# Performance work log

Hardware: AMD Instinct MI355X
Metric: run time of the kernel (lower is better)

## Reference

```python
import jax, jax.numpy as jnp
import numpy as np

C = 256
CQK = C // 8  # 32


def setup_inputs() -> dict:
    key = jax.random.key(0)
    ks = jax.random.split(key, 7)
    x = jax.random.normal(ks[0], (4, C, 64, 64), dtype=jnp.float32)
    s = 1.0 / np.sqrt(C)
    Wq = jax.random.normal(ks[1], (CQK, C), dtype=jnp.float32) * s
    bq = jnp.zeros((CQK,), dtype=jnp.float32)
    Wk = jax.random.normal(ks[2], (CQK, C), dtype=jnp.float32) * s
    bk = jnp.zeros((CQK,), dtype=jnp.float32)
    Wv = jax.random.normal(ks[3], (C, C), dtype=jnp.float32) * s
    bv = jnp.zeros((C,), dtype=jnp.float32)
    return {"x": x, "Wq": Wq, "bq": bq, "Wk": Wk, "bk": bk, "Wv": Wv, "bv": bv}


def reference(x, Wq, bq, Wk, bk, Wv, bv):
    B, Cc, H, W = x.shape
    xf = x.reshape(B, Cc, H * W)  # [B, C, HW]
    # 1x1 convs == per-pixel linear projections over channels
    q = jnp.einsum('oc,bcn->bno', Wq, xf) + bq          # [B, HW, C//8]
    k = jnp.einsum('oc,bcn->bon', Wk, xf) + bk[:, None]  # [B, C//8, HW]
    v = jnp.einsum('oc,bcn->bno', Wv, xf) + bv          # [B, HW, C]
    attn = jax.nn.softmax(jnp.einsum('bnd,bdm->bnm', q, k), axis=-1)  # [B, HW, HW]
    out = jnp.einsum('bnm,bmc->bnc', attn, v)           # [B, HW, C]
    return out.transpose(0, 2, 1).reshape(B, Cc, H, W)
```

## Files before the change

kernel.cpp:

```cpp
#include <hip/hip_runtime.h>
#include <hip/hip_bf16.h>


#define N_PIX 4096
#define DQK   32
#define CCH   256
#define LOG2E 1.44269504088896f

typedef __attribute__((ext_vector_type(8))) _Float16 f16x8;
typedef __attribute__((ext_vector_type(4))) _Float16 f16x4;
typedef __attribute__((ext_vector_type(2))) _Float16 f16x2;
typedef __attribute__((ext_vector_type(8))) short    bf16x8;
typedef __attribute__((ext_vector_type(4))) short    bf16x4;
typedef __attribute__((ext_vector_type(4))) float    f32x4;

__device__ inline void barrier_lds() {
    asm volatile("" ::: "memory");
    __builtin_amdgcn_s_waitcnt(0xc07f);
    __builtin_amdgcn_s_barrier();
    asm volatile("" ::: "memory");
}

__device__ inline unsigned cvt_pk_bf16(float lo, float hi) {
    unsigned r;
    asm("v_cvt_pk_bf16_f32 %0, %1, %2" : "=v"(r) : "v"(lo), "v"(hi));
    return r;
}

__global__ __launch_bounds__(256) void wpack_kernel(
    const float* __restrict__ Wq, const float* __restrict__ Wk,
    const float* __restrict__ Wv, _Float16* __restrict__ Wp)
{
    const int tid   = threadIdx.x;
    const int wflat = blockIdx.x * 4 + (tid >> 6);
    const int lane  = tid & 63;
    const int L15   = lane & 15;
    const int quad  = lane >> 4;
    const int mt    = wflat >> 3;
    const int ks    = wflat & 7;
    const int m0    = mt * 16;

    const float* Wsrc; int row; float scale = 1.f;
    if (m0 < 32)      { Wsrc = Wq; row = m0 + L15;      scale = LOG2E; }
    else if (m0 < 64) { Wsrc = Wk; row = m0 - 32 + L15; }
    else              { Wsrc = Wv; row = m0 - 64 + L15; }

    const float* p = Wsrc + (size_t)row * 256 + ks * 32 + quad * 8;
    f16x8 h;
    #pragma unroll
    for (int j = 0; j < 8; ++j) h[j] = (_Float16)(p[j] * scale);
    *(f16x8*)(Wp + ((size_t)wflat * 64 + lane) * 8) = h;
}

__global__ __launch_bounds__(640, 5) void qkv_kernel(
    const float* __restrict__ x, const _Float16* __restrict__ Wp,
    const float* __restrict__ bq, const float* __restrict__ bk,
    const float* __restrict__ bv,
    _Float16* __restrict__ qo, _Float16* __restrict__ ko,
    __hip_bfloat16* __restrict__ vp)
{
    __shared__ alignas(16) unsigned char shraw[256 * 40 * 2];
    _Float16       (*xT)[264] = (_Float16 (*)[264])shraw;
    __hip_bfloat16 (*vst)[40] = (__hip_bfloat16 (*)[40])shraw;

    const int idx = blockIdx.x;
    const int b   = (idx & 7) >> 1;
    const int n0  = (((idx >> 3) << 1) | (idx & 1)) * 32;
    const int tid = threadIdx.x;

    {
        const float* xb = x + (size_t)b * CCH * N_PIX;
        #pragma unroll
        for (int pass = 0; pass < 2; ++pass) {
            const int slot = pass * 640 + tid;
            if (slot < 1024) {
                const int c2 = (slot >> 3) * 2;
                const int n4 = (slot & 7) * 4;
                const float4 r0 = *(const float4*)(xb + (size_t)c2       * N_PIX + n0 + n4);
                const float4 r1 = *(const float4*)(xb + (size_t)(c2 + 1) * N_PIX + n0 + n4);
                const float a[4] = {r0.x, r0.y, r0.z, r0.w};
                const float c[4] = {r1.x, r1.y, r1.z, r1.w};
                #pragma unroll
                for (int i = 0; i < 4; ++i)
                    *(f16x2*)(&xT[n4 + i][c2]) = (f16x2){(_Float16)a[i], (_Float16)c[i]};
            }
        }
    }
    __syncthreads();

    const int lane = tid & 63;
    const int wid  = tid >> 6;
    const int L15  = lane & 15;
    const int quad = lane >> 4;

    const f32x4 fz = {0.f, 0.f, 0.f, 0.f};
    f32x4 acc[2][2];
    #pragma unroll
    for (int j = 0; j < 2; ++j) { acc[j][0] = fz; acc[j][1] = fz; }

    const _Float16* wpw = Wp + ((size_t)(wid * 2) * 8 * 64 + lane) * 8;

    #pragma unroll
    for (int ks = 0; ks < 8; ++ks) {
        const f16x8 a0 = *(const f16x8*)(wpw + (size_t)(0 * 8 + ks) * 512);
        const f16x8 a1 = *(const f16x8*)(wpw + (size_t)(1 * 8 + ks) * 512);
        #pragma unroll
        for (int nf = 0; nf < 2; ++nf) {
            const f16x8 bfr = *(const f16x8*)(&xT[nf * 16 + L15][ks * 32 + quad * 8]);
            acc[0][nf] = __builtin_amdgcn_mfma_f32_16x16x32_f16(a0, bfr, acc[0][nf], 0, 0, 0);
            acc[1][nf] = __builtin_amdgcn_mfma_f32_16x16x32_f16(a1, bfr, acc[1][nf], 0, 0, 0);
        }
    }

    #pragma unroll
    for (int j = 0; j < 2; ++j) {
        const int m0 = (wid * 2 + j) * 16;
        if (m0 < 32) {
            const int mr = m0 + quad * 4;
            #pragma unroll
            for (int nf = 0; nf < 2; ++nf) {
                const int n = n0 + nf * 16 + L15;
                f16x4 h;
                #pragma unroll
                for (int r = 0; r < 4; ++r) h[r] = (_Float16)(acc[j][nf][r] + bq[mr + r] * LOG2E);
                *(f16x4*)(qo + ((size_t)b * N_PIX + n) * DQK + mr) = h;
            }
        } else if (m0 < 64) {
            const int mr = m0 - 32 + quad * 4;
            #pragma unroll
            for (int nf = 0; nf < 2; ++nf) {
                const int n = n0 + nf * 16 + L15;
                f16x4 h;
                #pragma unroll
                for (int r = 0; r < 4; ++r) h[r] = (_Float16)(acc[j][nf][r] + bk[mr + r]);
                *(f16x4*)(ko + ((size_t)b * N_PIX + n) * DQK + mr) = h;
            }
        }
    }

    __syncthreads();

    #pragma unroll
    for (int j = 0; j < 2; ++j) {
        const int m0 = (wid * 2 + j) * 16;
        if (m0 >= 64) {
            const int c = m0 - 64 + quad * 4;
            #pragma unroll
            for (int nf = 0; nf < 2; ++nf) {
                const int np = nf * 16 + L15;
                #pragma unroll
                for (int r = 0; r < 4; ++r)
                    vst[c + r][np] = __float2bfloat16(acc[j][nf][r] + bv[c + r]);
            }
        }
    }
    __syncthreads();

    {
        __hip_bfloat16* vpb = vp + (size_t)b * 2048 * 512 + (size_t)((n0 >> 5) * 16) * 512;
        #pragma unroll
        for (int s = 0; s < 2; ++s) {
            const int slot = s * 640 + tid;
            if (slot < 1024) {
                const int cg16 = slot >> 6;
                const int ln   = slot & 63;
                const int qd   = ln >> 4;
                const int l15  = ln & 15;
                const bf16x8 val = *(const bf16x8*)(&vst[cg16 * 16 + l15][qd * 8]);
                *(bf16x8*)(vpb + ((size_t)cg16 * 64 + ln) * 8) = val;
            }
        }
    }
}


#define PV_BODY(J, VR)                                                            \
  {                                                                               \
    const int buf_ = (J) & 1;                                                     \
    _Pragma("unroll")                                                             \
    for (int qq_ = 0; qq_ < 4; ++qq_) {                                           \
      _Pragma("unroll")                                                           \
      for (int kk_ = 0; kk_ < 2; ++kk_) {                                         \
        const bf16x8 ap_ = *(const bf16x8*)(&Ps[buf_][qq_ * 2 + kk_][quad][L15][0]); \
        oacc[qq_][0] = __builtin_amdgcn_mfma_f32_16x16x32_bf16(                   \
            ap_, VR[kk_][0], oacc[qq_][0], 0, 0, 0);                              \
        oacc[qq_][1] = __builtin_amdgcn_mfma_f32_16x16x32_bf16(                   \
            ap_, VR[kk_][1], oacc[qq_][1], 0, 0, 0);                              \
      }                                                                           \
    }                                                                             \
    const __hip_bfloat16* vt_ = vb + (size_t)(((J) + 2) & 63) * 16384;            \
    _Pragma("unroll")                                                             \
    for (int kk_ = 0; kk_ < 2; ++kk_)                                             \
      _Pragma("unroll")                                                           \
      for (int cf_ = 0; cf_ < 2; ++cf_)                                           \
        VR[kk_][cf_] = *(const bf16x8*)(vt_ + voff0 + kk_ * 8192 + cf_ * 512);    \
  }

#define S_BODY(J, KR, DO_S)                                                       \
  {                                                                               \
    if (DO_S) {                                                                   \
      const int bufw_ = ((J) & 1) ^ 1;                                            \
      const f32x4 s0_ = __builtin_amdgcn_mfma_f32_16x16x32_f16(KR, aq0, fz, 0, 0, 0); \
      const f32x4 s1_ = __builtin_amdgcn_mfma_f32_16x16x32_f16(KR, aq1, fz, 0, 0, 0); \
      const _Float16* kp_ = kbp + (size_t)(((J) + 3) & 63) * (64 * DQK);          \
      KR = *(const f16x8*)(kp_ + koff);                                           \
      const float a0_ = exp2f(s0_[0]), a1_ = exp2f(s0_[1]);                       \
      const float a2_ = exp2f(s0_[2]), a3_ = exp2f(s0_[3]);                       \
      psum0 += (a0_ + a1_) + (a2_ + a3_);                                         \
      uint2 w0_; w0_.x = cvt_pk_bf16(a0_, a1_); w0_.y = cvt_pk_bf16(a2_, a3_);    \
      *(uint2*)(&Ps[bufw_][g0][s8][L15][e4]) = w0_;                               \
      const float b0_ = exp2f(s1_[0]), b1_ = exp2f(s1_[1]);                       \
      const float b2_ = exp2f(s1_[2]), b3_ = exp2f(s1_[3]);                       \
      psum1 += (b0_ + b1_) + (b2_ + b3_);                                         \
      uint2 w1_; w1_.x = cvt_pk_bf16(b0_, b1_); w1_.y = cvt_pk_bf16(b2_, b3_);    \
      *(uint2*)(&Ps[bufw_][g1][s8][L15][e4]) = w1_;                               \
    }                                                                             \
  }

__global__ __launch_bounds__(1024, 4) void attn_kernel(
    const _Float16* __restrict__ qg,
    const _Float16* __restrict__ kg,
    const __hip_bfloat16* __restrict__ vp,
    float* __restrict__ out)
{
    __shared__ __hip_bfloat16 Ps[2][8][4][16][8];
    __shared__ float lsum[4][4][16];

    const int idx  = blockIdx.x;
    const int b    = (idx & 7) >> 1;
    const int n0   = (((idx >> 3) << 1) | (idx & 1)) * 64;
    const int tid  = threadIdx.x;
    const int wid  = tid >> 6;
    const int lane = tid & 63;
    const int L15  = lane & 15;
    const int quad = lane >> 4;
    const bool is_pv = (wid < 8);

    const f32x4 fz = {0.f, 0.f, 0.f, 0.f};

    const int cg = wid & 7;
    const __hip_bfloat16* vb = vp + (size_t)b * 2048 * 512;
    const int voff0 = lane * 8 + cg * 2 * 512;
    f32x4 oacc[4][2];
    #pragma unroll
    for (int qq = 0; qq < 4; ++qq) { oacc[qq][0] = fz; oacc[qq][1] = fz; }
    bf16x8 vA[2][2], vB[2][2];

    const int skt = wid & 3;
    const int h   = (wid >> 2) & 1;
    const int g0  = 4 * h + (skt >> 1);
    const int g1  = g0 + 2;
    const int s8  = (skt & 1) * 2 + (quad >> 1);
    const int e4  = (quad & 1) * 4;
    const _Float16* kbp = kg + (size_t)b * N_PIX * DQK;
    const int koff = (skt * 16 + L15) * DQK + quad * 8;
    f16x8 aq0{}, aq1{}, kA{}, kB{};
    float psum0 = 0.f, psum1 = 0.f;

    if (is_pv) {
        #pragma unroll
        for (int kk = 0; kk < 2; ++kk)
            #pragma unroll
            for (int cf = 0; cf < 2; ++cf) {
                vA[kk][cf] = *(const bf16x8*)(vb +         voff0 + kk * 8192 + cf * 512);
                vB[kk][cf] = *(const bf16x8*)(vb + 16384 + voff0 + kk * 8192 + cf * 512);
            }
    } else {
        aq0 = *(const f16x8*)(qg + ((size_t)b * N_PIX + n0 + (2 * h + 0) * 16 + L15) * DQK + quad * 8);
        aq1 = *(const f16x8*)(qg + ((size_t)b * N_PIX + n0 + (2 * h + 1) * 16 + L15) * DQK + quad * 8);
        const f16x8 k00 = *(const f16x8*)(kbp + koff);
        kA = *(const f16x8*)(kbp + (size_t)1 * 64 * DQK + koff);
        kB = *(const f16x8*)(kbp + (size_t)2 * 64 * DQK + koff);
        const f32x4 s0 = __builtin_amdgcn_mfma_f32_16x16x32_f16(k00, aq0, fz, 0, 0, 0);
        const f32x4 s1 = __builtin_amdgcn_mfma_f32_16x16x32_f16(k00, aq1, fz, 0, 0, 0);
        const float a0 = exp2f(s0[0]), a1 = exp2f(s0[1]);
        const float a2 = exp2f(s0[2]), a3 = exp2f(s0[3]);
        psum0 += (a0 + a1) + (a2 + a3);
        uint2 w0; w0.x = cvt_pk_bf16(a0, a1); w0.y = cvt_pk_bf16(a2, a3);
        *(uint2*)(&Ps[0][g0][s8][L15][e4]) = w0;
        const float b0 = exp2f(s1[0]), b1 = exp2f(s1[1]);
        const float b2 = exp2f(s1[2]), b3 = exp2f(s1[3]);
        psum1 += (b0 + b1) + (b2 + b3);
        uint2 w1; w1.x = cvt_pk_bf16(b0, b1); w1.y = cvt_pk_bf16(b2, b3);
        *(uint2*)(&Ps[0][g1][s8][L15][e4]) = w1;
    }
    barrier_lds();

    for (int it = 0; it < 64; it += 2) {
        if (is_pv) { PV_BODY(it, vA) } else { S_BODY(it, kA, true) }
        barrier_lds();
        if (is_pv) { PV_BODY(it + 1, vB) } else { S_BODY(it + 1, kB, it < 62) }
        barrier_lds();
    }

    if (!is_pv) {
        psum0 += __shfl_xor(psum0, 16, 64);
        psum0 += __shfl_xor(psum0, 32, 64);
        psum1 += __shfl_xor(psum1, 16, 64);
        psum1 += __shfl_xor(psum1, 32, 64);
        if (quad == 0) {
            lsum[2 * h + 0][skt][L15] = psum0;
            lsum[2 * h + 1][skt][L15] = psum1;
        }
    }
    __syncthreads();

    if (is_pv) {
        float* ob = out + (size_t)b * CCH * N_PIX;
        #pragma unroll
        for (int qq = 0; qq < 4; ++qq) {
            float inv_l[4];
            #pragma unroll
            for (int r = 0; r < 4; ++r) {
                const int q = quad * 4 + r;
                inv_l[r] = 1.f / (lsum[qq][0][q] + lsum[qq][1][q] +
                                  lsum[qq][2][q] + lsum[qq][3][q]);
            }
            #pragma unroll
            for (int cf = 0; cf < 2; ++cf) {
                const int c = cg * 32 + cf * 16 + L15;
                f32x4 o;
                #pragma unroll
                for (int r = 0; r < 4; ++r) o[r] = oacc[qq][cf][r] * inv_l[r];
                *(f32x4*)(ob + (size_t)c * N_PIX + n0 + qq * 16 + quad * 4) = o;
            }
        }
    }
}

extern "C" void kernel_launch(void* const* d_in, const int* in_sizes, int n_in,
                              void* d_out, int out_size, void* d_ws, size_t ws_size,
                              hipStream_t stream) {
    (void)in_sizes; (void)n_in; (void)out_size; (void)ws_size;
    const float* x  = (const float*)d_in[0];
    const float* Wq = (const float*)d_in[1];
    const float* bq = (const float*)d_in[2];
    const float* Wk = (const float*)d_in[3];
    const float* bk = (const float*)d_in[4];
    const float* Wv = (const float*)d_in[5];
    const float* bv = (const float*)d_in[6];

    _Float16* qb = (_Float16*)d_ws;
    _Float16* kb = qb + (size_t)4 * N_PIX * DQK;
    __hip_bfloat16* vpk = (__hip_bfloat16*)(kb + (size_t)4 * N_PIX * DQK);
    _Float16* wp = (_Float16*)(vpk + (size_t)4 * 2048 * 512);
    float* outp = (float*)d_out;

    wpack_kernel<<<40, 256, 0, stream>>>(Wq, Wk, Wv, wp);
    qkv_kernel<<<512, 640, 0, stream>>>(x, wp, bq, bk, bv, qb, kb, vpk);
    attn_kernel<<<256, 1024, 0, stream>>>(qb, kb, vpk, outp);
}
```

Measured before the change: 135.6 us.

## Halve attention block to 8 waves with each wave doing twice the work

Shrinks the attention block from 16 waves to 8: four PV waves now each cover 64 channels (four column fragments), and four S waves each compute scores for all four 16-query tiles. The per-step work per wave doubles while the number of waves taking part in each LDS barrier halves. The goal is to cut barrier and sync overhead and to reuse each loaded P or K fragment across more MFMAs. The cost is higher register pressure (more accumulators and prefetched V fragments) and less latency hiding, since each CU has fewer waves.

```diff
diff --git a/kernel.cpp b/kernel.cpp
--- a/kernel.cpp
+++ b/kernel.cpp
@@ -182,18 +182,27 @@
       _Pragma("unroll")                                                           \
       for (int kk_ = 0; kk_ < 2; ++kk_) {                                         \
         const bf16x8 ap_ = *(const bf16x8*)(&Ps[buf_][qq_ * 2 + kk_][quad][L15][0]); \
-        oacc[qq_][0] = __builtin_amdgcn_mfma_f32_16x16x32_bf16(                   \
-            ap_, VR[kk_][0], oacc[qq_][0], 0, 0, 0);                              \
-        oacc[qq_][1] = __builtin_amdgcn_mfma_f32_16x16x32_bf16(                   \
-            ap_, VR[kk_][1], oacc[qq_][1], 0, 0, 0);                              \
+        _Pragma("unroll")                                                         \
+        for (int cf_ = 0; cf_ < 4; ++cf_)                                         \
+          oacc[qq_][cf_] = __builtin_amdgcn_mfma_f32_16x16x32_bf16(               \
+              ap_, VR[kk_][cf_], oacc[qq_][cf_], 0, 0, 0);                        \
       }                                                                           \
     }                                                                             \
     const __hip_bfloat16* vt_ = vb + (size_t)(((J) + 2) & 63) * 16384;            \
     _Pragma("unroll")                                                             \
     for (int kk_ = 0; kk_ < 2; ++kk_)                                             \
       _Pragma("unroll")                                                           \
-      for (int cf_ = 0; cf_ < 2; ++cf_)                                           \
+      for (int cf_ = 0; cf_ < 4; ++cf_)                                           \
         VR[kk_][cf_] = *(const bf16x8*)(vt_ + voff0 + kk_ * 8192 + cf_ * 512);    \
+  }
+
+#define S_QT(SACC, PSUM, QT, BUFW)                                                \
+  {                                                                               \
+    const float a0_ = exp2f(SACC[0]), a1_ = exp2f(SACC[1]);                       \
+    const float a2_ = exp2f(SACC[2]), a3_ = exp2f(SACC[3]);                       \
+    PSUM += (a0_ + a1_) + (a2_ + a3_);                                            \
+    uint2 w_; w_.x = cvt_pk_bf16(a0_, a1_); w_.y = cvt_pk_bf16(a2_, a3_);         \
+    *(uint2*)(&Ps[BUFW][(QT) * 2 + kh][s8][L15][e4]) = w_;                        \
   }
 
 #define S_BODY(J, KR, DO_S)                                                       \
@@ -202,22 +211,18 @@
       const int bufw_ = ((J) & 1) ^ 1;                                            \
       const f32x4 s0_ = __builtin_amdgcn_mfma_f32_16x16x32_f16(KR, aq0, fz, 0, 0, 0); \
       const f32x4 s1_ = __builtin_amdgcn_mfma_f32_16x16x32_f16(KR, aq1, fz, 0, 0, 0); \
+      const f32x4 s2_ = __builtin_amdgcn_mfma_f32_16x16x32_f16(KR, aq2, fz, 0, 0, 0); \
+      const f32x4 s3_ = __builtin_amdgcn_mfma_f32_16x16x32_f16(KR, aq3, fz, 0, 0, 0); \
       const _Float16* kp_ = kbp + (size_t)(((J) + 3) & 63) * (64 * DQK);          \
       KR = *(const f16x8*)(kp_ + koff);                                           \
-      const float a0_ = exp2f(s0_[0]), a1_ = exp2f(s0_[1]);                       \
-      const float a2_ = exp2f(s0_[2]), a3_ = exp2f(s0_[3]);                       \
-      psum0 += (a0_ + a1_) + (a2_ + a3_);                                         \
-      uint2 w0_; w0_.x = cvt_pk_bf16(a0_, a1_); w0_.y = cvt_pk_bf16(a2_, a3_);    \
-      *(uint2*)(&Ps[bufw_][g0][s8][L15][e4]) = w0_;                               \
-      const float b0_ = exp2f(s1_[0]), b1_ = exp2f(s1_[1]);                       \
-      const float b2_ = exp2f(s1_[2]), b3_ = exp2f(s1_[3]);                       \
-      psum1 += (b0_ + b1_) + (b2_ + b3_);                                         \
-      uint2 w1_; w1_.x = cvt_pk_bf16(b0_, b1_); w1_.y = cvt_pk_bf16(b2_, b3_);    \
-      *(uint2*)(&Ps[bufw_][g1][s8][L15][e4]) = w1_;                               \
+      S_QT(s0_, psum0, 0, bufw_)                                                  \
+      S_QT(s1_, psum1, 1, bufw_)                                                  \
+      S_QT(s2_, psum2, 2, bufw_)                                                  \
+      S_QT(s3_, psum3, 3, bufw_)                                                  \
     }                                                                             \
   }
 
-__global__ __launch_bounds__(1024, 4) void attn_kernel(
+__global__ __launch_bounds__(512, 2) void attn_kernel(
     const _Float16* __restrict__ qg,
     const _Float16* __restrict__ kg,
     const __hip_bfloat16* __restrict__ vp,
@@ -234,55 +239,54 @@
     const int lane = tid & 63;
     const int L15  = lane & 15;
     const int quad = lane >> 4;
-    const bool is_pv = (wid < 8);
+    const bool is_pv = (wid < 4);
 
     const f32x4 fz = {0.f, 0.f, 0.f, 0.f};
 
-    const int cg = wid & 7;
+    const int cg = wid & 3;
     const __hip_bfloat16* vb = vp + (size_t)b * 2048 * 512;
-    const int voff0 = lane * 8 + cg * 2 * 512;
-    f32x4 oacc[4][2];
-    #pragma unroll
-    for (int qq = 0; qq < 4; ++qq) { oacc[qq][0] = fz; oacc[qq][1] = fz; }
-    bf16x8 vA[2][2], vB[2][2];
+    const int voff0 = lane * 8 + cg * 4 * 512;
+    f32x4 oacc[4][4];
+    #pragma unroll
+    for (int qq = 0; qq < 4; ++qq)
+        #pragma unroll
+        for (int cf = 0; cf < 4; ++cf) oacc[qq][cf] = fz;
+    bf16x8 vA[2][4], vB[2][4];
 
     const int skt = wid & 3;
-    const int h   = (wid >> 2) & 1;
-    const int g0  = 4 * h + (skt >> 1);
-    const int g1  = g0 + 2;
+    const int kh  = skt >> 1;
     const int s8  = (skt & 1) * 2 + (quad >> 1);
     const int e4  = (quad & 1) * 4;
     const _Float16* kbp = kg + (size_t)b * N_PIX * DQK;
     const int koff = (skt * 16 + L15) * DQK + quad * 8;
-    f16x8 aq0{}, aq1{}, kA{}, kB{};
-    float psum0 = 0.f, psum1 = 0.f;
+    f16x8 aq0{}, aq1{}, aq2{}, aq3{}, kA{}, kB{};
+    float psum0 = 0.f, psum1 = 0.f, psum2 = 0.f, psum3 = 0.f;
 
     if (is_pv) {
         #pragma unroll
         for (int kk = 0; kk < 2; ++kk)
             #pragma unroll
-            for (int cf = 0; cf < 2; ++cf) {
+            for (int cf = 0; cf < 4; ++cf) {
                 vA[kk][cf] = *(const bf16x8*)(vb +         voff0 + kk * 8192 + cf * 512);
                 vB[kk][cf] = *(const bf16x8*)(vb + 16384 + voff0 + kk * 8192 + cf * 512);
             }
     } else {
-        aq0 = *(const f16x8*)(qg + ((size_t)b * N_PIX + n0 + (2 * h + 0) * 16 + L15) * DQK + quad * 8);
-        aq1 = *(const f16x8*)(qg + ((size_t)b * N_PIX + n0 + (2 * h + 1) * 16 + L15) * DQK + quad * 8);
+        const _Float16* qbase = qg + ((size_t)b * N_PIX + n0 + L15) * DQK + quad * 8;
+        aq0 = *(const f16x8*)(qbase + (size_t)(0 * 16) * DQK);
+        aq1 = *(const f16x8*)(qbase + (size_t)(1 * 16) * DQK);
+        aq2 = *(const f16x8*)(qbase + (size_t)(2 * 16) * DQK);
+        aq3 = *(const f16x8*)(qbase + (size_t)(3 * 16) * DQK);
         const f16x8 k00 = *(const f16x8*)(kbp + koff);
         kA = *(const f16x8*)(kbp + (size_t)1 * 64 * DQK + koff);
         kB = *(const f16x8*)(kbp + (size_t)2 * 64 * DQK + koff);
         const f32x4 s0 = __builtin_amdgcn_mfma_f32_16x16x32_f16(k00, aq0, fz, 0, 0, 0);
         const f32x4 s1 = __builtin_amdgcn_mfma_f32_16x16x32_f16(k00, aq1, fz, 0, 0, 0);
-        const float a0 = exp2f(s0[0]), a1 = exp2f(s0[1]);
-        const float a2 = exp2f(s0[2]), a3 = exp2f(s0[3]);
-        psum0 += (a0 + a1) + (a2 + a3);
-        uint2 w0; w0.x = cvt_pk_bf16(a0, a1); w0.y = cvt_pk_bf16(a2, a3);
-        *(uint2*)(&Ps[0][g0][s8][L15][e4]) = w0;
-        const float b0 = exp2f(s1[0]), b1 = exp2f(s1[1]);
-        const float b2 = exp2f(s1[2]), b3 = exp2f(s1[3]);
-        psum1 += (b0 + b1) + (b2 + b3);
-        uint2 w1; w1.x = cvt_pk_bf16(b0, b1); w1.y = cvt_pk_bf16(b2, b3);
-        *(uint2*)(&Ps[0][g1][s8][L15][e4]) = w1;
+        const f32x4 s2 = __builtin_amdgcn_mfma_f32_16x16x32_f16(k00, aq2, fz, 0, 0, 0);
+        const f32x4 s3 = __builtin_amdgcn_mfma_f32_16x16x32_f16(k00, aq3, fz, 0, 0, 0);
+        S_QT(s0, psum0, 0, 0)
+        S_QT(s1, psum1, 1, 0)
+        S_QT(s2, psum2, 2, 0)
+        S_QT(s3, psum3, 3, 0)
     }
     barrier_lds();
 
@@ -298,9 +302,15 @@
         psum0 += __shfl_xor(psum0, 32, 64);
         psum1 += __shfl_xor(psum1, 16, 64);
         psum1 += __shfl_xor(psum1, 32, 64);
+        psum2 += __shfl_xor(psum2, 16, 64);
+        psum2 += __shfl_xor(psum2, 32, 64);
+        psum3 += __shfl_xor(psum3, 16, 64);
+        psum3 += __shfl_xor(psum3, 32, 64);
         if (quad == 0) {
-            lsum[2 * h + 0][skt][L15] = psum0;
-            lsum[2 * h + 1][skt][L15] = psum1;
+            lsum[0][skt][L15] = psum0;
+            lsum[1][skt][L15] = psum1;
+            lsum[2][skt][L15] = psum2;
+            lsum[3][skt][L15] = psum3;
         }
     }
     __syncthreads();
@@ -317,8 +327,8 @@
                                   lsum[qq][2][q] + lsum[qq][3][q]);
             }
             #pragma unroll
-            for (int cf = 0; cf < 2; ++cf) {
-                const int c = cg * 32 + cf * 16 + L15;
+            for (int cf = 0; cf < 4; ++cf) {
+                const int c = cg * 64 + cf * 16 + L15;
                 f32x4 o;
                 #pragma unroll
                 for (int r = 0; r < 4; ++r) o[r] = oacc[qq][cf][r] * inv_l[r];
@@ -348,5 +358,5 @@
 
     wpack_kernel<<<40, 256, 0, stream>>>(Wq, Wk, Wv, wp);
     qkv_kernel<<<512, 640, 0, stream>>>(x, wp, bq, bk, bv, qb, kb, vpk);
-    attn_kernel<<<256, 1024, 0, stream>>>(qb, kb, vpk, outp);
-}
+    attn_kernel<<<256, 512, 0, stream>>>(qb, kb, vpk, outp);
+}
```

Result: no change. 137.0 us (+1.0%).
